# Kernel tuning notes

Measured on AMD Instinct MI355X. Metric: run time of the kernel, lower is better.

## Reference

```python
import jax, jax.numpy as jnp
import numpy as np
from jax import lax

V = 23       # vocab size (prime -> all nonzero scales invertible mod V)
H = 256      # hidden width of the strictly-causal masked layer
B, L = 512, 1024
TEMP = 1.0

_a = np.arange(V)
# one_hot_minus: out[k] = sum_a x[a] * shift[(a - k) % V]
MINUS_IDX = jnp.asarray((_a[None, :] - _a[:, None]) % V)  # [k, a] -> index into shift
# one_hot_multiply: T[s, k, a] = 1 if (s * a) % V == k
MUL_T = jnp.asarray(np.equal.outer(np.outer(_a, _a) % V, _a).transpose(0, 2, 1).astype(np.float32))  # [s, k, a]
# multiplicative inverse mod V (Fermat: s^(V-2) mod V for prime V); inv(0) := 0
_inv = np.array([pow(int(s), V - 2, V) if s else 0 for s in range(V)])
INV_P = jnp.asarray((_inv[:, None] == _a[None, :]).astype(np.float32))  # [s, k]


def one_hot_argmax(x, temp):
    """Straight-through one-hot argmax (soft = softmax(x/temp))."""
    soft = jax.nn.softmax(x / temp, axis=-1)
    hard = jax.nn.one_hot(jnp.argmax(x, axis=-1), V, dtype=x.dtype)
    return soft + lax.stop_gradient(hard - soft)


def one_hot_minus(x, shift):
    # (x - shift) % V in one-hot space: out[k] = sum_a x[a] * shift[(a-k)%V]
    return jnp.einsum('ba,bka->bk', x, shift[:, MINUS_IDX])


def one_hot_multiply(x, scale):
    # (x * scale) % V in one-hot space
    return jnp.einsum('bs,ba,ska->bk', scale, x, MUL_T)


def setup_inputs() -> dict:
    key = jax.random.key(0)
    k1, k2, k3 = jax.random.split(key, 3)
    x_tokens = jax.random.randint(k1, (B, L), 0, V, dtype=jnp.int32)
    W1 = jax.random.normal(k2, (V, H), jnp.float32) * 0.1
    b1 = jnp.zeros((H,), jnp.float32)
    W2 = jax.random.normal(k3, (H, 2 * V), jnp.float32) * 0.1
    b2 = jnp.zeros((2 * V,), jnp.float32)
    return {"x_tokens": x_tokens, "W1": W1, "b1": b1, "W2": W2, "b2": b2}


def reference(x_tokens, W1, b1, W2, b2):
    x = jax.nn.one_hot(x_tokens, V, dtype=jnp.float32)  # [B, L, V] one-hot inputs

    def step(acc, x_t):
        # acc [B, V] = sum of previously generated one-hot outputs y[0..t-1];
        # this is exactly what the strictly-causal layer sees at position t,
        # so net_t equals layer(padded_inputs)[:, t, :] of the original loop.
        net = jax.nn.relu(acc @ W1 + b1) @ W2 + b2      # [B, 2V]
        loc = one_hot_argmax(net[:, :V], TEMP)
        scale = one_hot_argmax(net[:, V:], TEMP)
        inv_scale = scale @ INV_P                        # one-hot modular inverse
        out_t = one_hot_multiply(one_hot_minus(x_t, loc), inv_scale)
        return acc + out_t, out_t

    acc0 = jnp.zeros((x.shape[0], V), x.dtype)
    _, ys = lax.scan(step, acc0, jnp.swapaxes(x, 0, 1))  # scan over length
    return jnp.swapaxes(ys, 0, 1)                        # [B, L, V]
```

## Files before the change

### kernel.cpp

```cpp
#include <hip/hip_runtime.h>
#include <math.h>

#define V 23
#define HH 256
#define BB 512
#define LL 1024
#define NOUT 46

constexpr unsigned long long packInv(int lo) {
    const int inv[23] = {0,1,12,8,6,14,4,10,3,18,7,21,2,16,5,20,13,19,9,17,15,11,22};
    unsigned long long t = 0;
    for (int i = 0; i < 12; ++i) {
        int idx = lo + i;
        if (idx < 23) t |= (unsigned long long)inv[idx] << (5 * i);
    }
    return t;
}
constexpr unsigned long long INV_T0 = packInv(0);
constexpr unsigned long long INV_T1 = packInv(12);

#define DPPMAX(v, ctrl, rmask)                                                  \
    do {                                                                        \
        unsigned _t = (unsigned)__builtin_amdgcn_update_dpp(                    \
            (int)(v), (int)(v), (ctrl), (rmask), 0xF, false);                   \
        (v) = ((v) > _t) ? (v) : _t;                                            \
    } while (0)

__global__ __launch_bounds__(256, 2)
void daf_kernel(const int* __restrict__ xtok,
                const float* __restrict__ W1,
                const float* __restrict__ b1,
                const float* __restrict__ W2,
                const float* __restrict__ b2,
                float* __restrict__ out)
{
    __shared__ float sW1[V * HH];
    __shared__ float sV[HH];
    __shared__ float sP[2][64][4];
    __shared__ int   sTok[LL];
    __shared__ int   sK[LL];

    const int tid = threadIdx.x;
    const int w   = tid >> 6;
    const int l   = tid & 63;
    const int b   = blockIdx.x;

    for (int i = tid; i < V * HH; i += 256) sW1[i] = W1[i];
    for (int i = tid; i < LL; i += 256) sTok[i] = xtok[(size_t)b * LL + i];

    const bool activeA = (l < V);
    const bool activeB = (l >= 32 && l < 32 + V);
    const bool active  = activeA || activeB;
    const int  col     = activeA ? l : (activeB ? (l - 32 + V) : 0);

    double h_pre = (double)b1[tid];

    const float bias = active ? b2[col] : 0.f;

    float wreg[64];
    #pragma unroll
    for (int ii = 0; ii < 64; ++ii)
        wreg[ii] = active ? W2[(size_t)(64 * w + ii) * NOUT + col] : 0.f;
    #pragma unroll
    for (int ii = 0; ii < 64; ++ii) asm volatile("" : "+v"(wreg[ii]));

    __syncthreads();

    for (int t = 0; t < LL; ++t) {
        const int tok = sTok[t];

        float v = fmaxf((float)h_pre, 0.f);
        sV[tid] = v;

        const float4* pv = (const float4*)(sV + 64 * w);
        float a0 = 0.f, a1 = 0.f, a2 = 0.f, a3 = 0.f;
        #pragma unroll
        for (int q = 0; q < 16; ++q) {
            float4 vv = pv[q];
            a0 = fmaf(vv.x, wreg[4 * q + 0], a0);
            a1 = fmaf(vv.y, wreg[4 * q + 1], a1);
            a2 = fmaf(vv.z, wreg[4 * q + 2], a2);
            a3 = fmaf(vv.w, wreg[4 * q + 3], a3);
        }
        const int p = t & 1;
        sP[p][l][w] = (a0 + a1) + (a2 + a3);
        __syncthreads();

        float4 ps = *(const float4*)&sP[p][l][0];
        float net = bias + ((ps.x + ps.y) + (ps.z + ps.w));
        int ib = __float_as_int(net);
        unsigned monoraw = (ib < 0) ? ~(unsigned)ib : ((unsigned)ib ^ 0x80000000u);
        const unsigned orig = active ? monoraw : 0u;

        unsigned red = orig;
        DPPMAX(red, 0xB1,  0xF);
        DPPMAX(red, 0x4E,  0xF);
        DPPMAX(red, 0x141, 0xF);
        DPPMAX(red, 0x140, 0xF);
        DPPMAX(red, 0x142, 0xA);
        const unsigned sA = (unsigned)__builtin_amdgcn_readlane((int)red, 16);
        const unsigned sB = (unsigned)__builtin_amdgcn_readlane((int)red, 48);

        const unsigned cmpv = (l < 32) ? sA : sB;
        const unsigned long long bal = __ballot(orig == cmpv);
        const int loc = __builtin_ctzll(bal & 0xFFFFFFFFull);
        const int sc  = __builtin_ctzll(bal >> 32);

        const unsigned long long tt = (sc < 12) ? INV_T0 : INV_T1;
        const int sh  = 5 * (sc - ((sc >= 12) ? 12 : 0));
        const int inv = (int)((tt >> sh) & 31);

        int m = tok - loc;
        m += (m >> 31) & V;
        const int k = (m * inv) % V;

        h_pre += (double)sW1[k * HH + tid];
        if (tid == 0) sK[t] = k;
    }

    __syncthreads();
    float* outb = out + (size_t)b * LL * V;
    for (int t = tid; t < LL; t += 256)
        outb[t * V + sK[t]] = 1.0f;
}

extern "C" void kernel_launch(void* const* d_in, const int* in_sizes, int n_in,
                              void* d_out, int out_size, void* d_ws, size_t ws_size,
                              hipStream_t stream) {
    const int*   xtok = (const int*)d_in[0];
    const float* W1   = (const float*)d_in[1];
    const float* b1   = (const float*)d_in[2];
    const float* W2   = (const float*)d_in[3];
    const float* b2   = (const float*)d_in[4];
    float* out = (float*)d_out;

    hipMemsetAsync(out, 0, (size_t)out_size * sizeof(float), stream);
    daf_kernel<<<BB, 256, 0, stream>>>(xtok, W1, b1, W2, b2, out);
}
```

Before: 779.3 us.

## Split hidden dimension across eight waves with 32 rows each

The block grows from 256 to 512 threads (8 waves), and each wave handles 32 hidden rows instead of 64. This halves the per-step serial FMA chain and the W2 register footprint per thread. Lanes 32-63 duplicate the h_pre state of lanes 0-31 so both vocab halves can be produced. In exchange the cross-wave reduction now reads 8 partials instead of 4, and the per-step barrier spans twice as many waves, which may raise sync cost and lower the number of resident blocks.

```diff
diff --git a/kernel.cpp b/kernel.cpp
--- a/kernel.cpp
+++ b/kernel.cpp
@@ -6,6 +6,8 @@
 #define BB 512
 #define LL 1024
 #define NOUT 46
+#define NW 8
+#define RPW 32
 
 constexpr unsigned long long packInv(int lo) {
     const int inv[23] = {0,1,12,8,6,14,4,10,3,18,7,21,2,16,5,20,13,19,9,17,15,11,22};
@@ -26,7 +28,7 @@
         (v) = ((v) > _t) ? (v) : _t;                                            \
     } while (0)
 
-__global__ __launch_bounds__(256, 2)
+__global__ __launch_bounds__(512, 4)
 void daf_kernel(const int* __restrict__ xtok,
                 const float* __restrict__ W1,
                 const float* __restrict__ b1,
@@ -35,34 +37,35 @@
                 float* __restrict__ out)
 {
     __shared__ float sW1[V * HH];
-    __shared__ float sV[HH];
-    __shared__ float sP[2][64][4];
+    __shared__ float sVw[NW][RPW];
+    __shared__ float sP[2][NW][64];
     __shared__ int   sTok[LL];
     __shared__ int   sK[LL];
 
-    const int tid = threadIdx.x;
-    const int w   = tid >> 6;
-    const int l   = tid & 63;
-    const int b   = blockIdx.x;
+    const int tid  = threadIdx.x;
+    const int w    = tid >> 6;
+    const int l    = tid & 63;
+    const int b    = blockIdx.x;
+    const int hrow = RPW * w + (l & (RPW - 1));
 
-    for (int i = tid; i < V * HH; i += 256) sW1[i] = W1[i];
-    for (int i = tid; i < LL; i += 256) sTok[i] = xtok[(size_t)b * LL + i];
+    for (int i = tid; i < V * HH; i += 512) sW1[i] = W1[i];
+    for (int i = tid; i < LL; i += 512) sTok[i] = xtok[(size_t)b * LL + i];
 
     const bool activeA = (l < V);
     const bool activeB = (l >= 32 && l < 32 + V);
     const bool active  = activeA || activeB;
     const int  col     = activeA ? l : (activeB ? (l - 32 + V) : 0);
 
-    double h_pre = (double)b1[tid];
+    double h_pre = (double)b1[hrow];
 
     const float bias = active ? b2[col] : 0.f;
 
-    float wreg[64];
+    float wreg[RPW];
     #pragma unroll
-    for (int ii = 0; ii < 64; ++ii)
-        wreg[ii] = active ? W2[(size_t)(64 * w + ii) * NOUT + col] : 0.f;
+    for (int ii = 0; ii < RPW; ++ii)
+        wreg[ii] = active ? W2[(size_t)(RPW * w + ii) * NOUT + col] : 0.f;
     #pragma unroll
-    for (int ii = 0; ii < 64; ++ii) asm volatile("" : "+v"(wreg[ii]));
+    for (int ii = 0; ii < RPW; ++ii) asm volatile("" : "+v"(wreg[ii]));
 
     __syncthreads();
 
@@ -70,12 +73,12 @@
         const int tok = sTok[t];
 
         float v = fmaxf((float)h_pre, 0.f);
-        sV[tid] = v;
+        sVw[w][l & (RPW - 1)] = v;
 
-        const float4* pv = (const float4*)(sV + 64 * w);
+        const float4* pv = (const float4*)sVw[w];
         float a0 = 0.f, a1 = 0.f, a2 = 0.f, a3 = 0.f;
         #pragma unroll
-        for (int q = 0; q < 16; ++q) {
+        for (int q = 0; q < 8; ++q) {
             float4 vv = pv[q];
             a0 = fmaf(vv.x, wreg[4 * q + 0], a0);
             a1 = fmaf(vv.y, wreg[4 * q + 1], a1);
@@ -83,11 +86,13 @@
             a3 = fmaf(vv.w, wreg[4 * q + 3], a3);
         }
         const int p = t & 1;
-        sP[p][l][w] = (a0 + a1) + (a2 + a3);
+        sP[p][w][l] = (a0 + a1) + (a2 + a3);
         __syncthreads();
 
-        float4 ps = *(const float4*)&sP[p][l][0];
-        float net = bias + ((ps.x + ps.y) + (ps.z + ps.w));
+        float s0 = sP[p][0][l], s1 = sP[p][1][l], s2 = sP[p][2][l], s3 = sP[p][3][l];
+        float s4 = sP[p][4][l], s5 = sP[p][5][l], s6 = sP[p][6][l], s7 = sP[p][7][l];
+        float net = bias + (((s0 + s1) + (s2 + s3)) + ((s4 + s5) + (s6 + s7)));
+
         int ib = __float_as_int(net);
         unsigned monoraw = (ib < 0) ? ~(unsigned)ib : ((unsigned)ib ^ 0x80000000u);
         const unsigned orig = active ? monoraw : 0u;
@@ -114,13 +119,13 @@
         m += (m >> 31) & V;
         const int k = (m * inv) % V;
 
-        h_pre += (double)sW1[k * HH + tid];
+        h_pre += (double)sW1[k * HH + hrow];
         if (tid == 0) sK[t] = k;
     }
 
     __syncthreads();
     float* outb = out + (size_t)b * LL * V;
-    for (int t = tid; t < LL; t += 256)
+    for (int t = tid; t < LL; t += 512)
         outb[t * V + sK[t]] = 1.0f;
 }
 
@@ -135,5 +140,5 @@
     float* out = (float*)d_out;
 
     hipMemsetAsync(out, 0, (size_t)out_size * sizeof(float), stream);
-    daf_kernel<<<BB, 256, 0, stream>>>(xtok, W1, b1, W2, b2, out);
+    daf_kernel<<<BB, 512, 0, stream>>>(xtok, W1, b1, W2, b2, out);
 }
```

Result: slower. 840.7 us (+7.9%).
